# Optimization experiments

Hardware: AMD Instinct MI355X
Metric: run time of the kernel (lower is better)

Reference implementation:

```python
import jax, jax.numpy as jnp
import numpy as np
import math

B, S, U, H = 2, 2048, 1024, 16
DK = U // H  # 64


def setup_inputs() -> dict:
    key = jax.random.key(0)
    ks = jax.random.split(key, 12)
    scale = 1.0 / math.sqrt(U)
    inp = {
        "query": jax.random.normal(ks[0], (B, S, U), dtype=jnp.float32),
        "key": jax.random.normal(ks[1], (B, S, U), dtype=jnp.float32),
        "value": jax.random.normal(ks[2], (B, S, U), dtype=jnp.float32),
        # causal mask, broadcast over batch: 1 = attend, 0 = masked
        "mask": jnp.broadcast_to(jnp.tril(jnp.ones((S, S), dtype=bool)), (B, S, S)),
        # nn.Linear params (torch convention: y = x @ W.T + b)
        "Wq": jax.random.uniform(ks[3], (U, U), jnp.float32, -scale, scale),
        "bq": jax.random.uniform(ks[4], (U,), jnp.float32, -scale, scale),
        "Wk": jax.random.uniform(ks[5], (U, U), jnp.float32, -scale, scale),
        "bk": jax.random.uniform(ks[6], (U,), jnp.float32, -scale, scale),
        "Wv": jax.random.uniform(ks[7], (U, U), jnp.float32, -scale, scale),
        "bv": jax.random.uniform(ks[8], (U,), jnp.float32, -scale, scale),
        "Wo": jax.random.uniform(ks[9], (U, U), jnp.float32, -scale, scale),
        "bo": jax.random.uniform(ks[10], (U,), jnp.float32, -scale, scale),
    }
    return inp


def reference(query, key, value, mask, Wq, bq, Wk, bk, Wv, bv, Wo, bo):
    b = query.shape[0]
    # QKV projections -> [b, H, S, DK]
    q = (query @ Wq.T + bq).reshape(b, -1, H, DK).transpose(0, 2, 1, 3)
    k = (key @ Wk.T + bk).reshape(b, -1, H, DK).transpose(0, 2, 1, 3)
    v = (value @ Wv.T + bv).reshape(b, -1, H, DK).transpose(0, 2, 1, 3)
    # scaled dot-product scores [b, H, Sq, Sk]
    scores = jnp.einsum("bhqd,bhkd->bhqk", q, k) / math.sqrt(DK)
    scores = jnp.where(mask[:, None, :, :], scores, jnp.float32(-1e9))
    A = jax.nn.softmax(scores, axis=-1)
    # dropout is eval/identity (p effectively inactive in reference)
    Hout = jnp.einsum("bhqk,bhkd->bhqd", A, v)
    H_concat = Hout.transpose(0, 2, 1, 3).reshape(b, -1, U)
    return H_concat @ Wo.T + bo
```

## Files before the change

kernel.cpp:

```cpp
#include <hip/hip_runtime.h>
#include <math.h>

#define B_NUM 2
#define S_LEN 2048
#define U_DIM 1024
#define H_NUM 16
#define DK 64
#define M_TOT (B_NUM * S_LEN)

typedef __attribute__((ext_vector_type(8))) short bf8;
typedef __attribute__((ext_vector_type(4))) float f4;

__device__ __forceinline__ unsigned short f2bf(float f) {
    union { float f; unsigned int u; } x; x.f = f;
    unsigned int r = x.u + 0x7fffu + ((x.u >> 16) & 1u);
    return (unsigned short)(r >> 16);
}

__device__ __forceinline__ void gl2lds16(const void* g, void* l) {
    __builtin_amdgcn_global_load_lds(
        (const __attribute__((address_space(1))) unsigned int*)g,
        (__attribute__((address_space(3))) unsigned int*)l, 16, 0, 0);
}

struct CvtArgs {
    const float* src[7];
    unsigned short* dst[7];
    int n[7];
};

__global__ __launch_bounds__(256) void convert_bf16(CvtArgs a)
{
    const int seg = blockIdx.y;
    const int i = (blockIdx.x * 256 + threadIdx.x) * 8;
    if (i >= a.n[seg]) return;
    const float* s = a.src[seg] + i;
    float4 v0 = *(const float4*)s;
    float4 v1 = *(const float4*)(s + 4);
    unsigned int p0 = (unsigned)f2bf(v0.x) | ((unsigned)f2bf(v0.y) << 16);
    unsigned int p1 = (unsigned)f2bf(v0.z) | ((unsigned)f2bf(v0.w) << 16);
    unsigned int p2 = (unsigned)f2bf(v1.x) | ((unsigned)f2bf(v1.y) << 16);
    unsigned int p3 = (unsigned)f2bf(v1.z) | ((unsigned)f2bf(v1.w) << 16);
    uint4 o = {p0, p1, p2, p3};
    *(uint4*)(a.dst[seg] + i) = o;
}

template <typename OutT>
__device__ __forceinline__ void gemm_core(
    const unsigned short* __restrict__ A, const unsigned short* __restrict__ W,
    const float* __restrict__ bias, OutT* __restrict__ C, float scale)
{
    __shared__ __align__(16) unsigned short As[2][128][32];
    __shared__ __align__(16) unsigned short Bs[2][128][32];

    const int tid = threadIdx.x;
    const int w = tid >> 6, lane = tid & 63;
    const int quad = lane >> 4, cid = lane & 15;
    const int wy = w >> 1, wx = w & 1;
    const int m0 = blockIdx.y * 128, n0 = blockIdx.x * 128;

    const int row_s = tid >> 1;
    const int sp = tid & 1;
    const int rr = (row_s >> 2) & 3;
    const int p0 = (2 * sp + rr) & 3;
    const int p1 = (2 * sp + 1 + rr) & 3;

    const unsigned short* gA = A + (size_t)(m0 + row_s) * U_DIM + 16 * sp;
    const unsigned short* gB = W + (size_t)(n0 + row_s) * U_DIM + 16 * sp;

    uint4 a0, a1, b0, b1;
#define GPF(k0_) do {                                   \
        a0 = *(const uint4*)(gA + (k0_));               \
        a1 = *(const uint4*)(gA + (k0_) + 8);           \
        b0 = *(const uint4*)(gB + (k0_));               \
        b1 = *(const uint4*)(gB + (k0_) + 8);           \
    } while (0)

    f4 acc[4][4] = {};

    GPF(0);
    *(uint4*)&As[0][row_s][p0 * 8] = a0;
    *(uint4*)&As[0][row_s][p1 * 8] = a1;
    *(uint4*)&Bs[0][row_s][p0 * 8] = b0;
    *(uint4*)&Bs[0][row_s][p1 * 8] = b1;
    GPF(32);
    __syncthreads();

#pragma unroll 2
    for (int k0 = 0; k0 < U_DIM; k0 += 32) {
        const int cur = (k0 >> 5) & 1;
        if (k0 + 32 < U_DIM) {
            const int nxt = cur ^ 1;
            *(uint4*)&As[nxt][row_s][p0 * 8] = a0;
            *(uint4*)&As[nxt][row_s][p1 * 8] = a1;
            *(uint4*)&Bs[nxt][row_s][p0 * 8] = b0;
            *(uint4*)&Bs[nxt][row_s][p1 * 8] = b1;
            if (k0 + 64 < U_DIM) GPF(k0 + 64);
        }

        bf8 af[4], bfr[4];
#pragma unroll
        for (int mt = 0; mt < 4; ++mt) {
            int row = wy * 64 + mt * 16 + cid;
            int seg = (quad + (row >> 2)) & 3;
            af[mt] = *(const bf8*)&As[cur][row][seg * 8];
        }
#pragma unroll
        for (int nt = 0; nt < 4; ++nt) {
            int row = wx * 64 + nt * 16 + cid;
            int seg = (quad + (row >> 2)) & 3;
            bfr[nt] = *(const bf8*)&Bs[cur][row][seg * 8];
        }
#pragma unroll
        for (int mt = 0; mt < 4; ++mt)
#pragma unroll
            for (int nt = 0; nt < 4; ++nt)
                acc[mt][nt] = __builtin_amdgcn_mfma_f32_16x16x32_bf16(
                    af[mt], bfr[nt], acc[mt][nt], 0, 0, 0);
        __syncthreads();
    }
#undef GPF

#pragma unroll
    for (int nt = 0; nt < 4; ++nt) {
        int col = n0 + wx * 64 + nt * 16 + cid;
        float bv = bias[col];
#pragma unroll
        for (int mt = 0; mt < 4; ++mt) {
            int rowb = m0 + wy * 64 + mt * 16 + quad * 4;
#pragma unroll
            for (int i = 0; i < 4; ++i) {
                float v = (acc[mt][nt][i] + bv) * scale;
                size_t idx = (size_t)(rowb + i) * U_DIM + col;
                if constexpr (sizeof(OutT) == 2) C[idx] = f2bf(v);
                else                             C[idx] = v;
            }
        }
    }
}

struct QkvArgs {
    const unsigned short* A[3];
    const unsigned short* W[3];
    const float* bias[3];
    unsigned short* C[3];
    float scale[3];
};

__global__ __launch_bounds__(256, 3) void gemm_qkv(QkvArgs a) {
    const int z = blockIdx.z;
    gemm_core<unsigned short>(a.A[z], a.W[z], a.bias[z], a.C[z], a.scale[z]);
}

__global__ __launch_bounds__(256, 3) void gemm_obf(
    const unsigned short* __restrict__ A, const unsigned short* __restrict__ W,
    const float* __restrict__ bias, float* __restrict__ C) {
    gemm_core<float>(A, W, bias, C, 1.0f);
}

__global__ __launch_bounds__(256) void transpose_v(
    const unsigned short* __restrict__ Vb, unsigned short* __restrict__ VT)
{
    __shared__ __align__(16) unsigned short tile[64][68];
    const int s0 = blockIdx.x * 64, h = blockIdx.y, b = blockIdx.z;
    const int tid = threadIdx.x;
    const int row = tid >> 3;
    const int sg = (tid & 7) * 8;
#pragma unroll
    for (int p = 0; p < 2; ++p) {
        int tok = p * 32 + row;
        const unsigned short* src = &Vb[((size_t)b * S_LEN + s0 + tok) * U_DIM + h * DK + sg];
        uint2 v0 = *(const uint2*)src;
        uint2 v1 = *(const uint2*)(src + 4);
        *(uint2*)&tile[tok][sg] = v0;
        *(uint2*)&tile[tok][sg + 4] = v1;
    }
    __syncthreads();
    const int lane = tid & 63, dg = tid >> 6;
    size_t obase = ((size_t)(b * H_NUM + h) * DK) * S_LEN + s0 + lane;
#pragma unroll
    for (int i = 0; i < 16; ++i) {
        int d = dg * 16 + i;
        VT[obase + (size_t)d * S_LEN] = tile[lane][d];
    }
}

__global__ __launch_bounds__(256, 3) void attn_mfma(
    const unsigned short* __restrict__ Q, const unsigned short* __restrict__ K,
    const unsigned short* __restrict__ VT, unsigned short* __restrict__ O)
{
    __shared__ __align__(16) unsigned short Ks[128][64];
    __shared__ __align__(16) unsigned short Vs[64][128];
    __shared__ __align__(16) unsigned short Ps[4][16][72];

    const int qt = (int)gridDim.x - 1 - (int)blockIdx.x;
    const int q0 = qt * 64;
    const int h = blockIdx.y, b = blockIdx.z;
    const int tid = threadIdx.x, w = tid >> 6, lane = tid & 63;
    const int quad = lane >> 4, cid = lane & 15;

#define KFRAG(r, s) (*(const bf8*)&Ks[r][(((s) ^ ((r) & 7)) * 8)])
#define VFRAG(r, s) (*(const bf8*)&Vs[r][(((((s) & 8) | (((s) ^ (r)) & 7))) * 8)])

    unsigned short (*QsA)[64] = (unsigned short (*)[64])&Ps[0][0][0];
    const int srow8 = lane >> 3;
    const int sw = ((lane & 7) ^ srow8) * 8;
    {
        const unsigned short* qg =
            Q + ((size_t)b * S_LEN + q0 + w * 16 + srow8) * U_DIM + h * DK + sw;
        gl2lds16(qg, &QsA[w * 16][0]);
        gl2lds16(qg + 8 * U_DIM, &QsA[w * 16 + 8][0]);
    }
    __syncthreads();
    const bf8 qfa = *(const bf8*)&QsA[w * 16 + cid][(((quad) ^ (cid & 7)) * 8)];
    const bf8 qfb = *(const bf8*)&QsA[w * 16 + cid][((((quad + 4)) ^ (cid & 7)) * 8)];

    const unsigned short* kgl =
        K + ((size_t)b * S_LEN + w * 32 + srow8) * U_DIM + h * DK + (lane & 7) * 8;
    const int vr0 = lane >> 4;
    const int s16 = lane & 15;
    const unsigned short* vgl =
        VT + ((size_t)(b * H_NUM + h) * DK + w * 16 + vr0) * S_LEN + s16 * 8;
    const int spE = (((s16 & 8) | ((s16 ^ vr0) & 7))) * 8;
    const int spO = (((s16 & 8) | ((s16 ^ (vr0 + 4)) & 7))) * 8;
    const int ksw = ((lane & 7) ^ srow8) * 8;

    uint4 kr0, kr1, kr2, kr3, vq0, vq1, vq2, vq3;
#define PREFETCH(kt_) do {                                                    \
        const unsigned short* kp_ = kgl + (size_t)(kt_) * 128 * U_DIM;        \
        kr0 = *(const uint4*)(kp_);                                           \
        kr1 = *(const uint4*)(kp_ + (size_t)8 * U_DIM);                       \
        kr2 = *(const uint4*)(kp_ + (size_t)16 * U_DIM);                      \
        kr3 = *(const uint4*)(kp_ + (size_t)24 * U_DIM);                      \
        const unsigned short* vp_ = vgl + (kt_) * 128;                        \
        vq0 = *(const uint4*)(vp_);                                           \
        vq1 = *(const uint4*)(vp_ + (size_t)4 * S_LEN);                       \
        vq2 = *(const uint4*)(vp_ + (size_t)8 * S_LEN);                       \
        vq3 = *(const uint4*)(vp_ + (size_t)12 * S_LEN);                      \
    } while (0)

    f4 o[4] = {};
    float l_i[4] = {0.0f, 0.0f, 0.0f, 0.0f};

    const int nkt = (qt >> 1) + 1;
    PREFETCH(0);

    for (int kt = 0; kt < nkt; ++kt) {
        __syncthreads();
        *(uint4*)&Ks[w * 32 + 0  + srow8][ksw] = kr0;
        *(uint4*)&Ks[w * 32 + 8  + srow8][ksw] = kr1;
        *(uint4*)&Ks[w * 32 + 16 + srow8][ksw] = kr2;
        *(uint4*)&Ks[w * 32 + 24 + srow8][ksw] = kr3;
        *(uint4*)&Vs[w * 16 + 0  + vr0][spE] = vq0;
        *(uint4*)&Vs[w * 16 + 4  + vr0][spO] = vq1;
        *(uint4*)&Vs[w * 16 + 8  + vr0][spE] = vq2;
        *(uint4*)&Vs[w * 16 + 12 + vr0][spO] = vq3;
        __syncthreads();
        if (kt + 1 < nkt) PREFETCH(kt + 1);

        f4 sc[8];
#pragma unroll
        for (int t = 0; t < 8; ++t) {
            int r = t * 16 + cid;
            f4 a = {};
            a = __builtin_amdgcn_mfma_f32_16x16x32_bf16(qfa, KFRAG(r, quad), a, 0, 0, 0);
            a = __builtin_amdgcn_mfma_f32_16x16x32_bf16(qfb, KFRAG(r, quad + 4), a, 0, 0, 0);
            sc[t] = a;
        }

        if (kt == nkt - 1) {
#pragma unroll
            for (int t = 0; t < 8; ++t) {
                int col = kt * 128 + t * 16 + cid;
#pragma unroll
                for (int i = 0; i < 4; ++i) {
                    int row = q0 + w * 16 + quad * 4 + i;
                    if (col > row) sc[t][i] = -1e30f;
                }
            }
        }

#pragma unroll
        for (int i = 0; i < 4; ++i) {
#pragma unroll
            for (int t = 0; t < 8; ++t) {
                float p = __expf(sc[t][i]);
                sc[t][i] = p;
                l_i[i] += p;
            }
        }

#pragma unroll
        for (int t = 0; t < 4; ++t)
#pragma unroll
            for (int i = 0; i < 4; ++i)
                Ps[w][quad * 4 + i][t * 16 + cid] = f2bf(sc[t][i]);
        {
            bf8 pA0 = *(const bf8*)&Ps[w][cid][quad * 8];
            bf8 pA1 = *(const bf8*)&Ps[w][cid][32 + quad * 8];
#pragma unroll
            for (int t = 0; t < 4; ++t) {
                int r = t * 16 + cid;
                o[t] = __builtin_amdgcn_mfma_f32_16x16x32_bf16(pA0, VFRAG(r, quad), o[t], 0, 0, 0);
                o[t] = __builtin_amdgcn_mfma_f32_16x16x32_bf16(pA1, VFRAG(r, 4 + quad), o[t], 0, 0, 0);
            }
        }
#pragma unroll
        for (int t = 0; t < 4; ++t)
#pragma unroll
            for (int i = 0; i < 4; ++i)
                Ps[w][quad * 4 + i][t * 16 + cid] = f2bf(sc[4 + t][i]);
        {
            bf8 pB0 = *(const bf8*)&Ps[w][cid][quad * 8];
            bf8 pB1 = *(const bf8*)&Ps[w][cid][32 + quad * 8];
#pragma unroll
            for (int t = 0; t < 4; ++t) {
                int r = t * 16 + cid;
                o[t] = __builtin_amdgcn_mfma_f32_16x16x32_bf16(pB0, VFRAG(r, 8 + quad), o[t], 0, 0, 0);
                o[t] = __builtin_amdgcn_mfma_f32_16x16x32_bf16(pB1, VFRAG(r, 12 + quad), o[t], 0, 0, 0);
            }
        }
    }
#undef PREFETCH
#undef KFRAG
#undef VFRAG

#pragma unroll
    for (int i = 0; i < 4; ++i) {
        float l = l_i[i];
        l += __shfl_xor(l, 1);
        l += __shfl_xor(l, 2);
        l += __shfl_xor(l, 4);
        l += __shfl_xor(l, 8);
        float inv = 1.0f / l;
        int rowg = q0 + w * 16 + quad * 4 + i;
        size_t rbase = ((size_t)b * S_LEN + rowg) * U_DIM + h * DK;
#pragma unroll
        for (int t = 0; t < 4; ++t)
            O[rbase + t * 16 + cid] = f2bf(o[t][i] * inv);
    }
}

extern "C" void kernel_launch(void* const* d_in, const int* in_sizes, int n_in,
                              void* d_out, int out_size, void* d_ws, size_t ws_size,
                              hipStream_t stream)
{
    const float* query = (const float*)d_in[0];
    const float* key   = (const float*)d_in[1];
    const float* value = (const float*)d_in[2];
    const float* Wq = (const float*)d_in[4];
    const float* bq = (const float*)d_in[5];
    const float* Wk = (const float*)d_in[6];
    const float* bk = (const float*)d_in[7];
    const float* Wv = (const float*)d_in[8];
    const float* bv = (const float*)d_in[9];
    const float* Wo = (const float*)d_in[10];
    const float* bo = (const float*)d_in[11];
    float* out = (float*)d_out;

    const size_t ACT = (size_t)M_TOT * U_DIM;
    const size_t WT  = (size_t)U_DIM * U_DIM;

    unsigned short* xq  = (unsigned short*)d_ws;
    unsigned short* xk  = xq + ACT;
    unsigned short* xv  = xk + ACT;
    unsigned short* wqb = xv + ACT;
    unsigned short* wkb = wqb + WT;
    unsigned short* wvb = wkb + WT;
    unsigned short* wob = wvb + WT;
    unsigned short* qg  = wob + WT;
    unsigned short* kg  = qg + ACT;
    unsigned short* vg  = kg + ACT;
    unsigned short* vt  = vg + ACT;
    unsigned short* ao  = vt + ACT;

    CvtArgs ca;
    ca.src[0] = query; ca.dst[0] = xq;  ca.n[0] = (int)ACT;
    ca.src[1] = key;   ca.dst[1] = xk;  ca.n[1] = (int)ACT;
    ca.src[2] = value; ca.dst[2] = xv;  ca.n[2] = (int)ACT;
    ca.src[3] = Wq;    ca.dst[3] = wqb; ca.n[3] = (int)WT;
    ca.src[4] = Wk;    ca.dst[4] = wkb; ca.n[4] = (int)WT;
    ca.src[5] = Wv;    ca.dst[5] = wvb; ca.n[5] = (int)WT;
    ca.src[6] = Wo;    ca.dst[6] = wob; ca.n[6] = (int)WT;
    convert_bf16<<<dim3(ACT / (256 * 8), 7), 256, 0, stream>>>(ca);

    QkvArgs ga;
    ga.A[0] = xq; ga.W[0] = wqb; ga.bias[0] = bq; ga.C[0] = qg; ga.scale[0] = 0.125f;
    ga.A[1] = xk; ga.W[1] = wkb; ga.bias[1] = bk; ga.C[1] = kg; ga.scale[1] = 1.0f;
    ga.A[2] = xv; ga.W[2] = wvb; ga.bias[2] = bv; ga.C[2] = vg; ga.scale[2] = 1.0f;
    gemm_qkv<<<dim3(U_DIM / 128, M_TOT / 128, 3), 256, 0, stream>>>(ga);

    transpose_v<<<dim3(S_LEN / 64, H_NUM, B_NUM), 256, 0, stream>>>(vg, vt);

    attn_mfma<<<dim3(S_LEN / 64, H_NUM, B_NUM), 256, 0, stream>>>(qg, kg, vt, ao);

    gemm_obf<<<dim3(U_DIM / 128, M_TOT / 128), 256, 0, stream>>>(ao, wob, bo, out);
}
```

Before: 267.5 us.

## Fuse V transpose into QKV GEMM epilogue, remap attention blocks per XCD, use exp2

The V projection GEMM now writes its output directly in the head-major transposed layout the attention kernel reads, so the separate transpose kernel and its extra pass over V are removed. The attention grid is remapped so each XCD handles a contiguous group of (batch, head) pairs while still scheduling heavy causal tiles first, aiming at better L2 reuse of K/V. The Q scale folds in log2(e) so the softmax can use exp2f instead of __expf. The transposed epilogue stores are strided by S_LEN and uncoalesced, which may slow the QKV GEMM.

```diff
diff --git a/kernel.cpp b/kernel.cpp
--- a/kernel.cpp
+++ b/kernel.cpp
@@ -45,10 +45,10 @@
     *(uint4*)(a.dst[seg] + i) = o;
 }
 
-template <typename OutT>
+template <int OMODE>
 __device__ __forceinline__ void gemm_core(
     const unsigned short* __restrict__ A, const unsigned short* __restrict__ W,
-    const float* __restrict__ bias, OutT* __restrict__ C, float scale)
+    const float* __restrict__ bias, void* __restrict__ Cv, float scale)
 {
     __shared__ __align__(16) unsigned short As[2][128][32];
     __shared__ __align__(16) unsigned short Bs[2][128][32];
@@ -131,9 +131,17 @@
 #pragma unroll
             for (int i = 0; i < 4; ++i) {
                 float v = (acc[mt][nt][i] + bv) * scale;
-                size_t idx = (size_t)(rowb + i) * U_DIM + col;
-                if constexpr (sizeof(OutT) == 2) C[idx] = f2bf(v);
-                else                             C[idx] = v;
+                if constexpr (OMODE == 0) {
+                    ((unsigned short*)Cv)[(size_t)(rowb + i) * U_DIM + col] = f2bf(v);
+                } else if constexpr (OMODE == 1) {
+                    ((float*)Cv)[(size_t)(rowb + i) * U_DIM + col] = v;
+                } else {
+                    int bb = rowb >> 11;
+                    int ss = (rowb & (S_LEN - 1)) + i;
+                    size_t idx = ((size_t)(bb * H_NUM + (col >> 6)) * DK + (col & 63))
+                                 * S_LEN + ss;
+                    ((unsigned short*)Cv)[idx] = f2bf(v);
+                }
             }
         }
     }
@@ -149,40 +157,16 @@
 
 __global__ __launch_bounds__(256, 3) void gemm_qkv(QkvArgs a) {
     const int z = blockIdx.z;
-    gemm_core<unsigned short>(a.A[z], a.W[z], a.bias[z], a.C[z], a.scale[z]);
+    if (z == 2)
+        gemm_core<2>(a.A[2], a.W[2], a.bias[2], a.C[2], a.scale[2]);
+    else
+        gemm_core<0>(a.A[z], a.W[z], a.bias[z], a.C[z], a.scale[z]);
 }
 
 __global__ __launch_bounds__(256, 3) void gemm_obf(
     const unsigned short* __restrict__ A, const unsigned short* __restrict__ W,
     const float* __restrict__ bias, float* __restrict__ C) {
-    gemm_core<float>(A, W, bias, C, 1.0f);
-}
-
-__global__ __launch_bounds__(256) void transpose_v(
-    const unsigned short* __restrict__ Vb, unsigned short* __restrict__ VT)
-{
-    __shared__ __align__(16) unsigned short tile[64][68];
-    const int s0 = blockIdx.x * 64, h = blockIdx.y, b = blockIdx.z;
-    const int tid = threadIdx.x;
-    const int row = tid >> 3;
-    const int sg = (tid & 7) * 8;
-#pragma unroll
-    for (int p = 0; p < 2; ++p) {
-        int tok = p * 32 + row;
-        const unsigned short* src = &Vb[((size_t)b * S_LEN + s0 + tok) * U_DIM + h * DK + sg];
-        uint2 v0 = *(const uint2*)src;
-        uint2 v1 = *(const uint2*)(src + 4);
-        *(uint2*)&tile[tok][sg] = v0;
-        *(uint2*)&tile[tok][sg + 4] = v1;
-    }
-    __syncthreads();
-    const int lane = tid & 63, dg = tid >> 6;
-    size_t obase = ((size_t)(b * H_NUM + h) * DK) * S_LEN + s0 + lane;
-#pragma unroll
-    for (int i = 0; i < 16; ++i) {
-        int d = dg * 16 + i;
-        VT[obase + (size_t)d * S_LEN] = tile[lane][d];
-    }
+    gemm_core<1>(A, W, bias, C, 1.0f);
 }
 
 __global__ __launch_bounds__(256, 3) void attn_mfma(
@@ -193,9 +177,16 @@
     __shared__ __align__(16) unsigned short Vs[64][128];
     __shared__ __align__(16) unsigned short Ps[4][16][72];
 
-    const int qt = (int)gridDim.x - 1 - (int)blockIdx.x;
+    const int L = (int)blockIdx.x + 32 * ((int)blockIdx.y + 16 * (int)blockIdx.z);
+    const int xcd = L & 7;
+    const int j   = L >> 3;
+    const int gl  = j & 3;
+    const int i   = j >> 2;
+    const int hb  = (xcd << 2) | gl;
+    const int h = hb & 15, b = hb >> 4;
+    const int qt = 31 - i;
+
     const int q0 = qt * 64;
-    const int h = blockIdx.y, b = blockIdx.z;
     const int tid = threadIdx.x, w = tid >> 6, lane = tid & 63;
     const int quad = lane >> 4, cid = lane & 15;
 
@@ -273,28 +264,28 @@
             for (int t = 0; t < 8; ++t) {
                 int col = kt * 128 + t * 16 + cid;
 #pragma unroll
-                for (int i = 0; i < 4; ++i) {
-                    int row = q0 + w * 16 + quad * 4 + i;
-                    if (col > row) sc[t][i] = -1e30f;
+                for (int i2 = 0; i2 < 4; ++i2) {
+                    int row = q0 + w * 16 + quad * 4 + i2;
+                    if (col > row) sc[t][i2] = -1e30f;
                 }
             }
         }
 
 #pragma unroll
-        for (int i = 0; i < 4; ++i) {
+        for (int i2 = 0; i2 < 4; ++i2) {
 #pragma unroll
             for (int t = 0; t < 8; ++t) {
-                float p = __expf(sc[t][i]);
-                sc[t][i] = p;
-                l_i[i] += p;
+                float p = exp2f(sc[t][i2]);
+                sc[t][i2] = p;
+                l_i[i2] += p;
             }
         }
 
 #pragma unroll
         for (int t = 0; t < 4; ++t)
 #pragma unroll
-            for (int i = 0; i < 4; ++i)
-                Ps[w][quad * 4 + i][t * 16 + cid] = f2bf(sc[t][i]);
+            for (int i2 = 0; i2 < 4; ++i2)
+                Ps[w][quad * 4 + i2][t * 16 + cid] = f2bf(sc[t][i2]);
         {
             bf8 pA0 = *(const bf8*)&Ps[w][cid][quad * 8];
             bf8 pA1 = *(const bf8*)&Ps[w][cid][32 + quad * 8];
@@ -308,8 +299,8 @@
 #pragma unroll
         for (int t = 0; t < 4; ++t)
 #pragma unroll
-            for (int i = 0; i < 4; ++i)
-                Ps[w][quad * 4 + i][t * 16 + cid] = f2bf(sc[4 + t][i]);
+            for (int i2 = 0; i2 < 4; ++i2)
+                Ps[w][quad * 4 + i2][t * 16 + cid] = f2bf(sc[4 + t][i2]);
         {
             bf8 pB0 = *(const bf8*)&Ps[w][cid][quad * 8];
             bf8 pB1 = *(const bf8*)&Ps[w][cid][32 + quad * 8];
@@ -326,18 +317,18 @@
 #undef VFRAG
 
 #pragma unroll
-    for (int i = 0; i < 4; ++i) {
-        float l = l_i[i];
+    for (int i2 = 0; i2 < 4; ++i2) {
+        float l = l_i[i2];
         l += __shfl_xor(l, 1);
         l += __shfl_xor(l, 2);
         l += __shfl_xor(l, 4);
         l += __shfl_xor(l, 8);
         float inv = 1.0f / l;
-        int rowg = q0 + w * 16 + quad * 4 + i;
+        int rowg = q0 + w * 16 + quad * 4 + i2;
         size_t rbase = ((size_t)b * S_LEN + rowg) * U_DIM + h * DK;
 #pragma unroll
         for (int t = 0; t < 4; ++t)
-            O[rbase + t * 16 + cid] = f2bf(o[t][i] * inv);
+            O[rbase + t * 16 + cid] = f2bf(o[t][i2] * inv);
     }
 }
 
@@ -385,13 +376,12 @@
     convert_bf16<<<dim3(ACT / (256 * 8), 7), 256, 0, stream>>>(ca);
 
     QkvArgs ga;
-    ga.A[0] = xq; ga.W[0] = wqb; ga.bias[0] = bq; ga.C[0] = qg; ga.scale[0] = 0.125f;
+    ga.A[0] = xq; ga.W[0] = wqb; ga.bias[0] = bq; ga.C[0] = qg;
+    ga.scale[0] = 0.125f * 1.44269504088896340736f;
     ga.A[1] = xk; ga.W[1] = wkb; ga.bias[1] = bk; ga.C[1] = kg; ga.scale[1] = 1.0f;
-    ga.A[2] = xv; ga.W[2] = wvb; ga.bias[2] = bv; ga.C[2] = vg; ga.scale[2] = 1.0f;
+    ga.A[2] = xv; ga.W[2] = wvb; ga.bias[2] = bv; ga.C[2] = vt; ga.scale[2] = 1.0f;
     gemm_qkv<<<dim3(U_DIM / 128, M_TOT / 128, 3), 256, 0, stream>>>(ga);
 
-    transpose_v<<<dim3(S_LEN / 64, H_NUM, B_NUM), 256, 0, stream>>>(vg, vt);
-
     attn_mfma<<<dim3(S_LEN / 64, H_NUM, B_NUM), 256, 0, stream>>>(qg, kg, vt, ao);
 
     gemm_obf<<<dim3(U_DIM / 128, M_TOT / 128), 256, 0, stream>>>(ao, wob, bo, out);
```

Result: faster. 251.4 us (-6.0%).
